# Kernel tuning notes

Measured on AMD Instinct MI355X. Metric: run time of the kernel, lower is better.

Reference implementation:

```python
import jax, jax.numpy as jnp
import numpy as np

DIM = 1024
NUM_HEADS = 16
HEAD_DIM = DIM // NUM_HEADS
HIDDEN = 2 * DIM  # swiglu hidden


def rotate_half(x):
    x1, x2 = jnp.split(x, 2, axis=-1)
    return jnp.concatenate((-x2, x1), axis=-1)


def setup_inputs() -> dict:
    key = jax.random.key(0)
    ks = jax.random.split(key, 9)
    s = lambda fan_in: 1.0 / np.sqrt(fan_in)
    x = jax.random.normal(ks[0], (4, 2048, DIM), dtype=jnp.float32)
    qkv_w = jax.random.uniform(ks[1], (3 * DIM, DIM), minval=-s(DIM), maxval=s(DIM))
    proj_w = jax.random.uniform(ks[2], (DIM, DIM), minval=-s(DIM), maxval=s(DIM))
    proj_b = jax.random.uniform(ks[3], (DIM,), minval=-s(DIM), maxval=s(DIM))
    w1_w = jax.random.uniform(ks[4], (HIDDEN, DIM), minval=-s(DIM), maxval=s(DIM))
    w1_b = jnp.zeros((HIDDEN,), jnp.float32)
    w2_w = jax.random.uniform(ks[5], (HIDDEN, DIM), minval=-s(DIM), maxval=s(DIM))
    w2_b = jnp.zeros((HIDDEN,), jnp.float32)
    w3_w = jax.random.uniform(ks[6], (DIM, HIDDEN), minval=-s(HIDDEN), maxval=s(HIDDEN))
    w3_b = jnp.zeros((DIM,), jnp.float32)
    return {"x": x, "qkv_w": qkv_w, "proj_w": proj_w, "proj_b": proj_b,
            "w1_w": w1_w, "w1_b": w1_b, "w2_w": w2_w, "w2_b": w2_b,
            "w3_w": w3_w, "w3_b": w3_b}


def reference(x, qkv_w, proj_w, proj_b, w1_w, w1_b, w2_w, w2_b, w3_w, w3_b):
    B, N, C = x.shape
    H, D = NUM_HEADS, HEAD_DIM
    scale = D ** -0.5
    # QKV projection (no bias)
    qkv = jnp.einsum('bnc,fc->bnf', x, qkv_w).reshape(B, N, 3, H, D)
    qkv = jnp.transpose(qkv, (2, 0, 3, 1, 4))  # [3, B, H, N, D]
    q, k, v = qkv[0], qkv[1], qkv[2]
    # Rotary embeddings
    inv_freq = 1.0 / (10000.0 ** (jnp.arange(0, D, 2, dtype=jnp.float32) / D))
    t = jnp.arange(N, dtype=jnp.float32)
    freqs = jnp.einsum('i,j->ij', t, inv_freq)
    emb = jnp.concatenate((freqs, freqs), axis=-1)[None, None]  # [1,1,N,D]
    cos, sin = jnp.cos(emb), jnp.sin(emb)
    q = q * cos + rotate_half(q) * sin
    k = k * cos + rotate_half(k) * sin
    # Attention (non-causal, as in source)
    attn = jnp.einsum('bhnd,bhmd->bhnm', q, k) * scale
    attn = jax.nn.softmax(attn, axis=-1)
    out = jnp.einsum('bhnm,bhmd->bhnd', attn, v)
    out = jnp.transpose(out, (0, 2, 1, 3)).reshape(B, N, C)
    out = jnp.einsum('bnc,fc->bnf', out, proj_w) + proj_b
    # SwiGLU MLP
    x1 = jnp.einsum('bnc,fc->bnf', out, w1_w) + w1_b
    x2 = jnp.einsum('bnc,fc->bnf', out, w2_w) + w2_b
    hidden = jax.nn.silu(x1) * x2
    return jnp.einsum('bnh,fh->bnf', hidden, w3_w) + w3_b
```

## Files before the change

kernel.cpp:

```cpp
#include <hip/hip_runtime.h>
#include <hip/hip_bf16.h>
#include <math.h>


#define SEQ     2048
#define BATCH   4
#define NH      16
#define CDIM    1024
#define MROWS   8192

typedef __bf16 bf16x8 __attribute__((ext_vector_type(8)));
typedef float  floatx4 __attribute__((ext_vector_type(4)));
typedef float  floatx16 __attribute__((ext_vector_type(16)));
typedef unsigned int u32;

__device__ __forceinline__ unsigned short f2bf(float f) {
    __bf16 h = (__bf16)f;
    return __builtin_bit_cast(unsigned short, h);
}
__device__ __forceinline__ float fexp2(float x) {
    float r; asm("v_exp_f32 %0, %1" : "=v"(r) : "v"(x)); return r;
}
__device__ __forceinline__ float frcp(float x) {
    float r; asm("v_rcp_f32 %0, %1" : "=v"(r) : "v"(x)); return r;
}
__device__ __forceinline__ u32 cvtpk(float lo, float hi) {
    u32 w; asm("v_cvt_pk_bf16_f32 %0, %1, %2" : "=v"(w) : "v"(lo), "v"(hi));
    return w;
}
__device__ __forceinline__ floatx4 mfma16(bf16x8 a, bf16x8 b, floatx4 c) {
    return __builtin_amdgcn_mfma_f32_16x16x32_bf16(a, b, c, 0, 0, 0);
}
__device__ __forceinline__ floatx16 mfma32(bf16x8 a, bf16x8 b, floatx16 c) {
    return __builtin_amdgcn_mfma_f32_32x32x16_bf16(a, b, c, 0, 0, 0);
}
__device__ __forceinline__ void gld16(void* lds, const void* g) {
    __builtin_amdgcn_global_load_lds(
        (const __attribute__((address_space(1))) u32*)g,
        (__attribute__((address_space(3))) u32*)lds, 16, 0, 0);
}
__device__ __forceinline__ void wait_vm0_barrier() {
    asm volatile("s_waitcnt vmcnt(0)" ::: "memory");
    __builtin_amdgcn_s_barrier();
    __builtin_amdgcn_sched_barrier(0);
}
__device__ __forceinline__ void raw_barrier() {
    __builtin_amdgcn_s_barrier();
    __builtin_amdgcn_sched_barrier(0);
}

template <int OUTMODE, bool BIAS>
__global__ __launch_bounds__(256) void mgemm(
    const unsigned short* __restrict__ A,
    const unsigned short* __restrict__ B,
    const float* __restrict__ bias,
    void* __restrict__ C, int ldc,
    int K)
{
    __shared__ __align__(16) unsigned short As[2][128 * 32];
    __shared__ __align__(16) unsigned short Bs[2][128 * 32];

    const int tid  = threadIdx.x;
    const int lane = tid & 63;
    const int wave = tid >> 6;
    const int l16  = lane & 15;
    const int quad = lane >> 4;
    const int wm = (wave >> 1) * 64, wn = (wave & 1) * 64;
    const int bm = blockIdx.y, bn = blockIdx.x;

    const unsigned short* Ag = A + (size_t)(bm * 128) * K;
    const unsigned short* Bg = B + (size_t)(bn * 128) * K;

    const int srow0 = wave * 32 + (lane >> 2);
    const int scol  = 8 * ((lane & 3) ^ ((lane >> 3) & 3));
    const unsigned short* gA0 = Ag + (size_t)srow0 * K + scol;
    const unsigned short* gA1 = Ag + (size_t)(srow0 + 16) * K + scol;
    const unsigned short* gB0 = Bg + (size_t)srow0 * K + scol;
    const unsigned short* gB1 = Bg + (size_t)(srow0 + 16) * K + scol;

    auto stage = [&](int b, int kt) {
        gld16(&As[b][(wave * 2 + 0) * 512], gA0 + kt);
        gld16(&As[b][(wave * 2 + 1) * 512], gA1 + kt);
        gld16(&Bs[b][(wave * 2 + 0) * 512], gB0 + kt);
        gld16(&Bs[b][(wave * 2 + 1) * 512], gB1 + kt);
    };

    const int qsw = (quad ^ ((l16 >> 1) & 3)) * 8;

    floatx4 acc[4][4] = {};
    const int NK = K >> 5;

    stage(0, 0);
    wait_vm0_barrier();

    for (int i = 0; i < NK; ++i) {
        const int cur = i & 1;
        if (i + 1 < NK) stage(cur ^ 1, (i + 1) * 32);

        bf16x8 af[4], bfr[4];
        #pragma unroll
        for (int mt = 0; mt < 4; ++mt)
            af[mt] = *(const bf16x8*)&As[cur][(wm + mt * 16 + l16) * 32 + qsw];
        #pragma unroll
        for (int nt = 0; nt < 4; ++nt)
            bfr[nt] = *(const bf16x8*)&Bs[cur][(wn + nt * 16 + l16) * 32 + qsw];
        #pragma unroll
        for (int mt = 0; mt < 4; ++mt)
            #pragma unroll
            for (int nt = 0; nt < 4; ++nt)
                acc[mt][nt] = mfma16(af[mt], bfr[nt], acc[mt][nt]);

        if (i + 1 < NK) wait_vm0_barrier();
        else            raw_barrier();
    }

    #pragma unroll
    for (int nt = 0; nt < 4; ++nt) {
        const int gcol = bn * 128 + wn + nt * 16 + l16;
        const float bv = BIAS ? bias[gcol] : 0.0f;
        #pragma unroll
        for (int mt = 0; mt < 4; ++mt) {
            #pragma unroll
            for (int r = 0; r < 4; ++r) {
                const int grow = bm * 128 + wm + mt * 16 + quad * 4 + r;
                float v = acc[mt][nt][r] + bv;
                if (OUTMODE == 0)
                    ((float*)C)[(size_t)grow * ldc + gcol] = v;
                else
                    ((unsigned short*)C)[(size_t)grow * ldc + gcol] = f2bf(v);
            }
        }
    }
}

#define RD_A(buf, mh)                                                     \
    { _Pragma("unroll") for (int i_ = 0; i_ < 4; ++i_) {                  \
        const int ro_ = (arow + ((mh) * 4 + i_) * 16) * 64;               \
        aF[i_][0] = *(const bf16x8*)&As[buf][ro_ + e0];                   \
        aF[i_][1] = *(const bf16x8*)&As[buf][ro_ + e1]; } }

#define RD_B(buf, nh)                                                     \
    { _Pragma("unroll") for (int n_ = 0; n_ < 2; ++n_) {                  \
        const int ro_ = (brow + ((nh) * 2 + n_) * 16) * 64;               \
        bF[nh][n_][0] = *(const bf16x8*)&Bs[buf][ro_ + e0];               \
        bF[nh][n_][1] = *(const bf16x8*)&Bs[buf][ro_ + e1]; } }

#define DO_MFMA(mh, nh)                                                   \
    { _Pragma("unroll") for (int i_ = 0; i_ < 4; ++i_)                    \
      { _Pragma("unroll") for (int n_ = 0; n_ < 2; ++n_) {                \
        acc[(mh)*4+i_][(nh)*2+n_] =                                       \
            mfma16(aF[i_][0], bF[nh][n_][0], acc[(mh)*4+i_][(nh)*2+n_]);  \
        acc[(mh)*4+i_][(nh)*2+n_] =                                       \
            mfma16(aF[i_][1], bF[nh][n_][1], acc[(mh)*4+i_][(nh)*2+n_]);  \
      } } }

#define PH_ENTER()                                                        \
    __builtin_amdgcn_s_barrier();                                         \
    asm volatile("s_waitcnt lgkmcnt(0)" ::: "memory");                    \
    __builtin_amdgcn_sched_barrier(0);                                    \
    __builtin_amdgcn_s_setprio(1)

#define PH_EXIT() __builtin_amdgcn_s_setprio(0)

#define EIGHT_PHASE_LOOP()                                                \
    stA(0, 0, 0); stA(0, 1, 0); stB(0, 0, 0); stB(0, 1, 0);               \
    stA(1, 0, 64);                                                        \
    asm volatile("s_waitcnt vmcnt(2)" ::: "memory");                      \
    __builtin_amdgcn_s_barrier();                                         \
    __builtin_amdgcn_sched_barrier(0);                                    \
    for (int j = 0; j < 8; ++j) {                                         \
        const int k1 = (2 * j + 1) * 64;                                  \
        const int k2 = (2 * j + 2) * 64;                                  \
        const int k3 = (2 * j + 3) * 64;                                  \
        const bool more = (j < 7);                                        \
        RD_A(0, 0); RD_B(0, 0);                                           \
        stA(1, 1, k1);                                                    \
        PH_ENTER(); DO_MFMA(0, 0); PH_EXIT();                             \
        __builtin_amdgcn_s_barrier();                                     \
        RD_B(0, 1);                                                       \
        stB(1, 0, k1);                                                    \
        PH_ENTER(); DO_MFMA(0, 1); PH_EXIT();                             \
        __builtin_amdgcn_s_barrier();                                     \
        RD_A(0, 1);                                                       \
        stB(1, 1, k1);                                                    \
        PH_ENTER(); DO_MFMA(1, 1); PH_EXIT();                             \
        __builtin_amdgcn_s_barrier();                                     \
        if (more) stA(0, 0, k2);                                          \
        PH_ENTER(); DO_MFMA(1, 0); PH_EXIT();                             \
        if (more) { asm volatile("s_waitcnt vmcnt(2)" ::: "memory"); }    \
        else      { asm volatile("s_waitcnt vmcnt(0)" ::: "memory"); }    \
        __builtin_amdgcn_s_barrier();                                     \
        RD_A(1, 0); RD_B(1, 0);                                           \
        if (more) stA(0, 1, k2);                                          \
        PH_ENTER(); DO_MFMA(0, 0); PH_EXIT();                             \
        __builtin_amdgcn_s_barrier();                                     \
        RD_B(1, 1);                                                       \
        if (more) stB(0, 0, k2);                                          \
        PH_ENTER(); DO_MFMA(0, 1); PH_EXIT();                             \
        __builtin_amdgcn_s_barrier();                                     \
        RD_A(1, 1);                                                       \
        if (more) stB(0, 1, k2);                                          \
        PH_ENTER(); DO_MFMA(1, 1); PH_EXIT();                             \
        __builtin_amdgcn_s_barrier();                                     \
        if (more) stA(1, 0, k3);                                          \
        PH_ENTER(); DO_MFMA(1, 0); PH_EXIT();                             \
        if (more) {                                                       \
            asm volatile("s_waitcnt vmcnt(2)" ::: "memory");              \
            __builtin_amdgcn_s_barrier();                                 \
        }                                                                 \
    }

__global__ __launch_bounds__(512, 2) void mgemm_glu(
    const unsigned short* __restrict__ B1p,
    const unsigned short* __restrict__ B2p,
    const unsigned short* __restrict__ A,
    const float* __restrict__ bias1,
    const float* __restrict__ bias2,
    unsigned short* __restrict__ C, int ldc)
{
    __shared__ __align__(16) unsigned short As[2][256 * 64];
    __shared__ __align__(16) unsigned short Bs[2][256 * 64];

    const int tid  = threadIdx.x;
    const int lane = tid & 63;
    const int wave = tid >> 6;
    const int l16  = lane & 15;
    const int quad = lane >> 4;
    const int wr   = wave >> 2;
    const int wc   = wave & 3;
    const int bn = blockIdx.x, bm = blockIdx.y;
    const int K = CDIM;

    const unsigned short* Ag = A + (size_t)(bm * 256) * K;

    const int srow  = lane >> 3;
    const int sgcol = ((lane & 7) ^ srow) * 8;

    auto stA = [&](int buf, int half, int kt) {
        #pragma unroll
        for (int s = 0; s < 2; ++s) {
            const int rbase = half * 128 + (wave * 2 + s) * 8;
            gld16(&As[buf][rbase * 64],
                  Ag + (size_t)(rbase + srow) * K + kt + sgcol);
        }
    };
    auto stB = [&](int buf, int half, int kt) {
        #pragma unroll
        for (int s = 0; s < 2; ++s) {
            const int rbase = half * 128 + (wave * 2 + s) * 8;
            const int q = rbase >> 6, r6 = rbase & 63;
            const unsigned short* src = (r6 < 32)
                ? B1p + (size_t)(bn * 128 + q * 32 + r6) * K
                : B2p + (size_t)(bn * 128 + q * 32 + (r6 - 32)) * K;
            gld16(&Bs[buf][rbase * 64],
                  src + (size_t)srow * K + kt + sgcol);
        }
    };

    const int e0 = ((quad)     ^ (l16 & 7)) * 8;
    const int e1 = ((quad + 4) ^ (l16 & 7)) * 8;
    const int arow = wr * 128 + l16;
    const int brow = wc * 64 + l16;

    floatx4 acc[8][4] = {};
    bf16x8 aF[4][2];
    bf16x8 bF[2][2][2];

    EIGHT_PHASE_LOOP();

    #pragma unroll
    for (int nt = 0; nt < 2; ++nt) {
        const int gcol = bn * 128 + wc * 32 + nt * 16 + l16;
        const float b1 = bias1[gcol];
        const float b2 = bias2[gcol];
        #pragma unroll
        for (int m = 0; m < 8; ++m) {
            #pragma unroll
            for (int r = 0; r < 4; ++r) {
                const int grow = bm * 256 + wr * 128 + m * 16 + quad * 4 + r;
                const float x1 = acc[m][nt][r] + b1;
                const float x2 = acc[m][nt + 2][r] + b2;
                const float e = fexp2(x1 * -1.44269504088896f);
                const float v = x1 * frcp(1.0f + e) * x2;
                C[(size_t)grow * ldc + gcol] = f2bf(v);
            }
        }
    }
}

__global__ __launch_bounds__(512, 2) void mgemm_qkv(
    const unsigned short* __restrict__ A,
    const unsigned short* __restrict__ B,
    const float* __restrict__ tab,
    unsigned short* __restrict__ Qb,
    unsigned short* __restrict__ Kb,
    unsigned short* __restrict__ Vtb)
{
    __shared__ __align__(16) unsigned short As[2][256 * 64];
    __shared__ __align__(16) unsigned short Bs[2][256 * 64];

    const int tid  = threadIdx.x;
    const int lane = tid & 63;
    const int wave = tid >> 6;
    const int l16  = lane & 15;
    const int quad = lane >> 4;
    const int wr   = wave >> 2;
    const int wc   = wave & 3;
    const int bn = blockIdx.x, bm = blockIdx.y;
    const int K = CDIM;

    const unsigned short* Ag = A + (size_t)(bm * 256) * K;
    const unsigned short* Bg = B + (size_t)(bn * 256) * K;

    const int srow  = lane >> 3;
    const int sgcol = ((lane & 7) ^ srow) * 8;

    auto stA = [&](int buf, int half, int kt) {
        #pragma unroll
        for (int s = 0; s < 2; ++s) {
            const int rbase = half * 128 + (wave * 2 + s) * 8;
            gld16(&As[buf][rbase * 64],
                  Ag + (size_t)(rbase + srow) * K + kt + sgcol);
        }
    };
    auto stB = [&](int buf, int half, int kt) {
        #pragma unroll
        for (int s = 0; s < 2; ++s) {
            const int rbase = half * 128 + (wave * 2 + s) * 8;
            gld16(&Bs[buf][rbase * 64],
                  Bg + (size_t)(rbase + srow) * K + kt + sgcol);
        }
    };

    const int e0 = ((quad)     ^ (l16 & 7)) * 8;
    const int e1 = ((quad + 4) ^ (l16 & 7)) * 8;
    const int arow = wr * 128 + l16;
    const int brow = wc * 64 + l16;

    floatx4 acc[8][4] = {};
    bf16x8 aF[4][2];
    bf16x8 bF[2][2][2];

    EIGHT_PHASE_LOOP();

    const int part = bn >> 2;

    if (part == 2) {
        unsigned short* T = &As[0][0];
        #pragma unroll
        for (int m = 0; m < 8; ++m) {
            __syncthreads();
            #pragma unroll
            for (int n = 0; n < 4; ++n) {
                ushort4 pk;
                pk.x = f2bf(acc[m][n][0]); pk.y = f2bf(acc[m][n][1]);
                pk.z = f2bf(acc[m][n][2]); pk.w = f2bf(acc[m][n][3]);
                *(ushort4*)&T[(wr * 256 + wc * 64 + n * 16 + l16) * 16 + quad * 4] = pk;
            }
            __syncthreads();
            const int wr2 = tid >> 8, col = tid & 255;
            const int grow0 = bm * 256 + wr2 * 128 + m * 16;
            const int b = grow0 >> 11, n0 = grow0 & 2047;
            const int h2 = (bn & 3) * 4 + (col >> 6);
            const int d  = col & 63;
            unsigned short* dst = Vtb +
                ((size_t)(b * NH + h2) * 64 + d) * 2048 + n0;
            const int tb = (wr2 * 256 + col) * 16;
            *(uint4*)dst       = *(const uint4*)&T[tb];
            *(uint4*)(dst + 8) = *(const uint4*)&T[tb + 8];
        }
    } else {
        const float qscale = (part == 0) ? 0.125f * 1.44269504088896f : 1.0f;
        const int h = (bn & 3) * 4 + wc;
        unsigned short* qk = (part == 0) ? Qb : Kb;
        #pragma unroll
        for (int m = 0; m < 8; ++m) {
            #pragma unroll
            for (int r = 0; r < 4; ++r) {
                const int grow = bm * 256 + wr * 128 + m * 16 + quad * 4 + r;
                const int b = grow >> 11, n = grow & 2047;
                unsigned short* dst = qk + ((size_t)(b * NH + h) * 2048 + n) * 64;
                #pragma unroll
                for (int nt = 0; nt < 2; ++nt) {
                    const int i = nt * 16 + l16;
                    const float c  = tab[(n * 32 + i) * 2];
                    const float sn = tab[(n * 32 + i) * 2 + 1];
                    const float x1  = acc[m][nt][r];
                    const float x2v = acc[m][nt + 2][r];
                    dst[i]      = f2bf((x1 * c - x2v * sn) * qscale);
                    dst[i + 32] = f2bf((x2v * c + x1 * sn) * qscale);
                }
            }
        }
    }
}

__global__ __launch_bounds__(256) void attn_mfma(
    const unsigned short* __restrict__ Qb,
    const unsigned short* __restrict__ Kb,
    const unsigned short* __restrict__ Vtb,
    unsigned short* __restrict__ Ob)
{
    const int bh = blockIdx.x;
    const int qt = blockIdx.y;
    const int tid = threadIdx.x;
    const int lane = tid & 63, wave = tid >> 6;
    const int r32 = lane & 31, hi = lane >> 5;
    const int qrow = wave * 32 + r32;

    __shared__ unsigned short QP[128][72];
    __shared__ unsigned short Ks[64][72];
    __shared__ unsigned short Vs[64][72];

    const unsigned short* Qg = Qb + ((size_t)bh * 2048 + qt * 128) * 64;
    const unsigned short* Kg = Kb + (size_t)bh * 2048 * 64;
    const unsigned short* Vg = Vtb + (size_t)bh * 64 * 2048;

    #pragma unroll
    for (int rep = 0; rep < 4; ++rep) {
        const int c = tid + rep * 256;
        const int r = c >> 3, d0 = (c & 7) * 8;
        *(uint4*)&QP[r][d0] = *(const uint4*)(Qg + (size_t)r * 64 + d0);
    }

    const int c0 = tid, c1 = tid + 256;
    const int kr0 = c0 >> 3, kd0 = (c0 & 7) * 8;
    const int kr1 = c1 >> 3, kd1 = (c1 & 7) * 8;

    uint4 ka0 = *(const uint4*)(Kg + (size_t)kr0 * 64 + kd0);
    uint4 ka1 = *(const uint4*)(Kg + (size_t)kr1 * 64 + kd1);
    uint4 va0 = *(const uint4*)(Vg + (size_t)kr0 * 2048 + kd0);
    uint4 va1 = *(const uint4*)(Vg + (size_t)kr1 * 2048 + kd1);

    __syncthreads();

    bf16x8 bq[4];
    #pragma unroll
    for (int f = 0; f < 4; ++f)
        bq[f] = *(const bf16x8*)&QP[qrow][f * 16 + hi * 8];

    floatx16 o0 = {}, o1 = {};
    float l_acc = 0.0f;

    for (int kt = 0; kt < 32; ++kt) {
        __syncthreads();
        *(uint4*)&Ks[kr0][kd0] = ka0;
        *(uint4*)&Ks[kr1][kd1] = ka1;
        *(uint4*)&Vs[kr0][kd0] = va0;
        *(uint4*)&Vs[kr1][kd1] = va1;
        if (kt + 1 < 32) {
            const size_t nb = (size_t)(kt + 1) * 64;
            ka0 = *(const uint4*)(Kg + (nb + kr0) * 64 + kd0);
            ka1 = *(const uint4*)(Kg + (nb + kr1) * 64 + kd1);
            va0 = *(const uint4*)(Vg + (size_t)kr0 * 2048 + nb + kd0);
            va1 = *(const uint4*)(Vg + (size_t)kr1 * 2048 + nb + kd1);
        }
        __syncthreads();

        #pragma unroll
        for (int t = 0; t < 2; ++t) {
            floatx16 s = {};
            #pragma unroll
            for (int f = 0; f < 4; ++f) {
                const bf16x8 ak = *(const bf16x8*)&Ks[t * 32 + r32][f * 16 + hi * 8];
                s = mfma32(ak, bq[f], s);
            }
            float p[16];
            float rs = 0.0f;
            #pragma unroll
            for (int g = 0; g < 16; ++g) { p[g] = fexp2(s[g]); rs += p[g]; }
            l_acc += rs;
            u32 w0 = cvtpk(p[0], p[1]),   w2 = cvtpk(p[4], p[5]);
            u32 w1 = cvtpk(p[2], p[3]),   w3 = cvtpk(p[6], p[7]);
            u32 w4 = cvtpk(p[8], p[9]),   w6 = cvtpk(p[12], p[13]);
            u32 w5 = cvtpk(p[10], p[11]), w7 = cvtpk(p[14], p[15]);
            asm("v_permlane32_swap_b32 %0, %1" : "+v"(w0), "+v"(w2));
            asm("v_permlane32_swap_b32 %0, %1" : "+v"(w1), "+v"(w3));
            asm("v_permlane32_swap_b32 %0, %1" : "+v"(w4), "+v"(w6));
            asm("v_permlane32_swap_b32 %0, %1" : "+v"(w5), "+v"(w7));
            uint4 u0; u0.x = w0; u0.y = w1; u0.z = w2; u0.w = w3;
            uint4 u1; u1.x = w4; u1.y = w5; u1.z = w6; u1.w = w7;
            const bf16x8 bp0 = __builtin_bit_cast(bf16x8, u0);
            const bf16x8 bp1 = __builtin_bit_cast(bf16x8, u1);
            {
                const int f0 = 2 * t, f1 = 2 * t + 1;
                const bf16x8 av00 = *(const bf16x8*)&Vs[r32][f0 * 16 + hi * 8];
                const bf16x8 av01 = *(const bf16x8*)&Vs[32 + r32][f0 * 16 + hi * 8];
                o0 = mfma32(av00, bp0, o0);
                o1 = mfma32(av01, bp0, o1);
                const bf16x8 av10 = *(const bf16x8*)&Vs[r32][f1 * 16 + hi * 8];
                const bf16x8 av11 = *(const bf16x8*)&Vs[32 + r32][f1 * 16 + hi * 8];
                o0 = mfma32(av10, bp1, o0);
                o1 = mfma32(av11, bp1, o1);
            }
        }
    }

    const float l_tot = l_acc + __shfl_xor(l_acc, 32);
    const float inv = 1.0f / l_tot;
    const int b = bh >> 4, h = bh & 15;
    unsigned short* orow = Ob +
        (size_t)(b * SEQ + qt * 128 + qrow) * CDIM + h * 64;
    #pragma unroll
    for (int u = 0; u < 2; ++u) {
        const floatx16 ov = u ? o1 : o0;
        #pragma unroll
        for (int g = 0; g < 4; ++g) {
            ushort4 pk;
            pk.x = f2bf(ov[4 * g + 0] * inv); pk.y = f2bf(ov[4 * g + 1] * inv);
            pk.z = f2bf(ov[4 * g + 2] * inv); pk.w = f2bf(ov[4 * g + 3] * inv);
            *(ushort4*)(orow + u * 32 + 8 * g + 4 * hi) = pk;
        }
    }
}

__global__ __launch_bounds__(256) void cvt_all(
    const float* __restrict__ x,    const float* __restrict__ qkv,
    const float* __restrict__ proj, const float* __restrict__ w1,
    const float* __restrict__ w2,   const float* __restrict__ w3,
    unsigned short* __restrict__ xb,    unsigned short* __restrict__ qkvb,
    unsigned short* __restrict__ projb, unsigned short* __restrict__ w1b,
    unsigned short* __restrict__ w2b,   unsigned short* __restrict__ w3b)
{
    const size_t i = ((size_t)blockIdx.x * 256 + threadIdx.x) * 4;
    const float* src; unsigned short* dst; size_t off;
    if      (i <  8388608) { src = x;    dst = xb;    off = 0; }
    else if (i < 11534336) { src = qkv;  dst = qkvb;  off = 8388608; }
    else if (i < 12582912) { src = proj; dst = projb; off = 11534336; }
    else if (i < 14680064) { src = w1;   dst = w1b;   off = 12582912; }
    else if (i < 16777216) { src = w2;   dst = w2b;   off = 14680064; }
    else                   { src = w3;   dst = w3b;   off = 16777216; }
    const size_t j = i - off;
    const float4 f = *(const float4*)(src + j);
    ushort4 o; o.x = f2bf(f.x); o.y = f2bf(f.y); o.z = f2bf(f.z); o.w = f2bf(f.w);
    *(ushort4*)(dst + j) = o;
}

__global__ __launch_bounds__(256) void rope_table(float* __restrict__ tab)
{
    const int idx = blockIdx.x * 256 + threadIdx.x;
    const int i = idx & 31, n = idx >> 5;
    const double f = (double)n * pow(10000.0, -(double)(2 * i) / 64.0);
    tab[idx * 2]     = (float)cos(f);
    tab[idx * 2 + 1] = (float)sin(f);
}

extern "C" void kernel_launch(void* const* d_in, const int* in_sizes, int n_in,
                              void* d_out, int out_size, void* d_ws, size_t ws_size,
                              hipStream_t stream)
{
    const float* x      = (const float*)d_in[0];
    const float* qkv_w  = (const float*)d_in[1];
    const float* proj_w = (const float*)d_in[2];
    const float* proj_b = (const float*)d_in[3];
    const float* w1_w   = (const float*)d_in[4];
    const float* w1_b   = (const float*)d_in[5];
    const float* w2_w   = (const float*)d_in[6];
    const float* w2_b   = (const float*)d_in[7];
    const float* w3_w   = (const float*)d_in[8];
    const float* w3_b   = (const float*)d_in[9];
    float* out = (float*)d_out;

    char* ws = (char*)d_ws;
    unsigned short* Qb    = (unsigned short*)(ws);
    unsigned short* Kb    = (unsigned short*)(ws + 16777216);
    unsigned short* Vtb   = (unsigned short*)(ws + 33554432);
    unsigned short* Ob    = (unsigned short*)(ws + 50331648);
    unsigned short* out1b = (unsigned short*)(ws + 67108864);
    unsigned short* w1b   = (unsigned short*)(ws + 83886080);
    unsigned short* w2b   = (unsigned short*)(ws + 88080384);
    unsigned short* w3b   = (unsigned short*)(ws + 92274688);
    unsigned short* projb = (unsigned short*)(ws + 96468992);
    unsigned short* xb    = (unsigned short*)(ws + 98566144);
    unsigned short* wqkvb = (unsigned short*)(ws + 115343360);
    float*          tab   = (float*)(ws + 121634816);
    unsigned short* hid   = (unsigned short*)(ws);

    const dim3 blk(256);

    cvt_all<<<dim3(18432), blk, 0, stream>>>(
        x, qkv_w, proj_w, w1_w, w2_w, w3_w,
        xb, wqkvb, projb, w1b, w2b, w3b);
    rope_table<<<dim3(256), blk, 0, stream>>>(tab);

    mgemm_qkv<<<dim3(12, 32), dim3(512), 0, stream>>>(xb, wqkvb, tab, Qb, Kb, Vtb);
    attn_mfma<<<dim3(BATCH * NH, SEQ / 128), blk, 0, stream>>>(Qb, Kb, Vtb, Ob);
    mgemm<1, true><<<dim3(8, 64), blk, 0, stream>>>(
        Ob, projb, proj_b, out1b, CDIM, CDIM);
    mgemm_glu<<<dim3(16, 32), dim3(512), 0, stream>>>(
        w1b, w2b, out1b, w1_b, w2_b, hid, 2048);
    mgemm<0, true><<<dim3(8, 64), blk, 0, stream>>>(
        hid, w3b, w3_b, out, CDIM, 2048);
}
```

Measured before the change: 422.8 us.

## Port proj and w3 GEMMs to 8-wave eight-phase pipelined kernel

Replaces the simple double-buffered 128x128 mgemm used for the output projection and final w3 GEMM with a 512-thread 256x128 tile kernel. The new kernel reuses the eight-phase staged-load/MFMA schedule already used by the GLU and QKV GEMMs, now with a configurable K trip count. The aim is to hide global-to-LDS latency and raise MFMA density. Separately, the attention kernel swaps __syncthreads for an explicit lgkmcnt wait plus barrier and raises wave priority around its MFMA groups. The larger tile halves the grid to 256 blocks, which may underfill the GPU's compute units.

```diff
diff --git a/kernel.cpp b/kernel.cpp
--- a/kernel.cpp
+++ b/kernel.cpp
@@ -39,99 +39,62 @@
         (const __attribute__((address_space(1))) u32*)g,
         (__attribute__((address_space(3))) u32*)lds, 16, 0, 0);
 }
-__device__ __forceinline__ void wait_vm0_barrier() {
-    asm volatile("s_waitcnt vmcnt(0)" ::: "memory");
-    __builtin_amdgcn_s_barrier();
-    __builtin_amdgcn_sched_barrier(0);
-}
-__device__ __forceinline__ void raw_barrier() {
-    __builtin_amdgcn_s_barrier();
-    __builtin_amdgcn_sched_barrier(0);
-}
-
-template <int OUTMODE, bool BIAS>
-__global__ __launch_bounds__(256) void mgemm(
-    const unsigned short* __restrict__ A,
-    const unsigned short* __restrict__ B,
-    const float* __restrict__ bias,
-    void* __restrict__ C, int ldc,
-    int K)
-{
-    __shared__ __align__(16) unsigned short As[2][128 * 32];
-    __shared__ __align__(16) unsigned short Bs[2][128 * 32];
-
-    const int tid  = threadIdx.x;
-    const int lane = tid & 63;
-    const int wave = tid >> 6;
-    const int l16  = lane & 15;
-    const int quad = lane >> 4;
-    const int wm = (wave >> 1) * 64, wn = (wave & 1) * 64;
-    const int bm = blockIdx.y, bn = blockIdx.x;
-
-    const unsigned short* Ag = A + (size_t)(bm * 128) * K;
-    const unsigned short* Bg = B + (size_t)(bn * 128) * K;
-
-    const int srow0 = wave * 32 + (lane >> 2);
-    const int scol  = 8 * ((lane & 3) ^ ((lane >> 3) & 3));
-    const unsigned short* gA0 = Ag + (size_t)srow0 * K + scol;
-    const unsigned short* gA1 = Ag + (size_t)(srow0 + 16) * K + scol;
-    const unsigned short* gB0 = Bg + (size_t)srow0 * K + scol;
-    const unsigned short* gB1 = Bg + (size_t)(srow0 + 16) * K + scol;
-
-    auto stage = [&](int b, int kt) {
-        gld16(&As[b][(wave * 2 + 0) * 512], gA0 + kt);
-        gld16(&As[b][(wave * 2 + 1) * 512], gA1 + kt);
-        gld16(&Bs[b][(wave * 2 + 0) * 512], gB0 + kt);
-        gld16(&Bs[b][(wave * 2 + 1) * 512], gB1 + kt);
-    };
-
-    const int qsw = (quad ^ ((l16 >> 1) & 3)) * 8;
-
-    floatx4 acc[4][4] = {};
-    const int NK = K >> 5;
-
-    stage(0, 0);
-    wait_vm0_barrier();
-
-    for (int i = 0; i < NK; ++i) {
-        const int cur = i & 1;
-        if (i + 1 < NK) stage(cur ^ 1, (i + 1) * 32);
-
-        bf16x8 af[4], bfr[4];
-        #pragma unroll
-        for (int mt = 0; mt < 4; ++mt)
-            af[mt] = *(const bf16x8*)&As[cur][(wm + mt * 16 + l16) * 32 + qsw];
-        #pragma unroll
-        for (int nt = 0; nt < 4; ++nt)
-            bfr[nt] = *(const bf16x8*)&Bs[cur][(wn + nt * 16 + l16) * 32 + qsw];
-        #pragma unroll
-        for (int mt = 0; mt < 4; ++mt)
-            #pragma unroll
-            for (int nt = 0; nt < 4; ++nt)
-                acc[mt][nt] = mfma16(af[mt], bfr[nt], acc[mt][nt]);
-
-        if (i + 1 < NK) wait_vm0_barrier();
-        else            raw_barrier();
-    }
-
-    #pragma unroll
-    for (int nt = 0; nt < 4; ++nt) {
-        const int gcol = bn * 128 + wn + nt * 16 + l16;
-        const float bv = BIAS ? bias[gcol] : 0.0f;
-        #pragma unroll
-        for (int mt = 0; mt < 4; ++mt) {
-            #pragma unroll
-            for (int r = 0; r < 4; ++r) {
-                const int grow = bm * 128 + wm + mt * 16 + quad * 4 + r;
-                float v = acc[mt][nt][r] + bv;
-                if (OUTMODE == 0)
-                    ((float*)C)[(size_t)grow * ldc + gcol] = v;
-                else
-                    ((unsigned short*)C)[(size_t)grow * ldc + gcol] = f2bf(v);
-            }
-        }
-    }
-}
+
+#define PH_ENTER()                                                        \
+    __builtin_amdgcn_s_barrier();                                         \
+    asm volatile("s_waitcnt lgkmcnt(0)" ::: "memory");                    \
+    __builtin_amdgcn_sched_barrier(0);                                    \
+    __builtin_amdgcn_s_setprio(1)
+
+#define PH_EXIT() __builtin_amdgcn_s_setprio(0)
+
+#define EIGHT_PHASE_LOOP(NJ)                                              \
+    stA(0, 0, 0); stA(0, 1, 0); stB(0, 0, 0); stB(0, 1, 0);               \
+    stA(1, 0, 64);                                                        \
+    asm volatile("s_waitcnt vmcnt(2)" ::: "memory");                      \
+    __builtin_amdgcn_s_barrier();                                         \
+    __builtin_amdgcn_sched_barrier(0);                                    \
+    for (int j = 0; j < (NJ); ++j) {                                      \
+        const int k1 = (2 * j + 1) * 64;                                  \
+        const int k2 = (2 * j + 2) * 64;                                  \
+        const int k3 = (2 * j + 3) * 64;                                  \
+        const bool more = (j < (NJ) - 1);                                 \
+        RD_A(0, 0); RD_B(0, 0);                                           \
+        stA(1, 1, k1);                                                    \
+        PH_ENTER(); DO_MFMA(0, 0); PH_EXIT();                             \
+        __builtin_amdgcn_s_barrier();                                     \
+        RD_B(0, 1);                                                       \
+        stB(1, 0, k1);                                                    \
+        PH_ENTER(); DO_MFMA(0, 1); PH_EXIT();                             \
+        __builtin_amdgcn_s_barrier();                                     \
+        RD_A(0, 1);                                                       \
+        stB(1, 1, k1);                                                    \
+        PH_ENTER(); DO_MFMA(1, 1); PH_EXIT();                             \
+        __builtin_amdgcn_s_barrier();                                     \
+        if (more) stA(0, 0, k2);                                          \
+        PH_ENTER(); DO_MFMA(1, 0); PH_EXIT();                             \
+        if (more) { asm volatile("s_waitcnt vmcnt(2)" ::: "memory"); }    \
+        else      { asm volatile("s_waitcnt vmcnt(0)" ::: "memory"); }    \
+        __builtin_amdgcn_s_barrier();                                     \
+        RD_A(1, 0); RD_B(1, 0);                                           \
+        if (more) stA(0, 1, k2);                                          \
+        PH_ENTER(); DO_MFMA(0, 0); PH_EXIT();                             \
+        __builtin_amdgcn_s_barrier();                                     \
+        RD_B(1, 1);                                                       \
+        if (more) stB(0, 0, k2);                                          \
+        PH_ENTER(); DO_MFMA(0, 1); PH_EXIT();                             \
+        __builtin_amdgcn_s_barrier();                                     \
+        RD_A(1, 1);                                                       \
+        if (more) stB(0, 1, k2);                                          \
+        PH_ENTER(); DO_MFMA(1, 1); PH_EXIT();                             \
+        __builtin_amdgcn_s_barrier();                                     \
+        if (more) stA(1, 0, k3);                                          \
+        PH_ENTER(); DO_MFMA(1, 0); PH_EXIT();                             \
+        if (more) {                                                       \
+            asm volatile("s_waitcnt vmcnt(2)" ::: "memory");              \
+            __builtin_amdgcn_s_barrier();                                 \
+        }                                                                 \
+    }
 
 #define RD_A(buf, mh)                                                     \
     { _Pragma("unroll") for (int i_ = 0; i_ < 4; ++i_) {                  \
@@ -153,62 +116,6 @@
         acc[(mh)*4+i_][(nh)*2+n_] =                                       \
             mfma16(aF[i_][1], bF[nh][n_][1], acc[(mh)*4+i_][(nh)*2+n_]);  \
       } } }
-
-#define PH_ENTER()                                                        \
-    __builtin_amdgcn_s_barrier();                                         \
-    asm volatile("s_waitcnt lgkmcnt(0)" ::: "memory");                    \
-    __builtin_amdgcn_sched_barrier(0);                                    \
-    __builtin_amdgcn_s_setprio(1)
-
-#define PH_EXIT() __builtin_amdgcn_s_setprio(0)
-
-#define EIGHT_PHASE_LOOP()                                                \
-    stA(0, 0, 0); stA(0, 1, 0); stB(0, 0, 0); stB(0, 1, 0);               \
-    stA(1, 0, 64);                                                        \
-    asm volatile("s_waitcnt vmcnt(2)" ::: "memory");                      \
-    __builtin_amdgcn_s_barrier();                                         \
-    __builtin_amdgcn_sched_barrier(0);                                    \
-    for (int j = 0; j < 8; ++j) {                                         \
-        const int k1 = (2 * j + 1) * 64;                                  \
-        const int k2 = (2 * j + 2) * 64;                                  \
-        const int k3 = (2 * j + 3) * 64;                                  \
-        const bool more = (j < 7);                                        \
-        RD_A(0, 0); RD_B(0, 0);                                           \
-        stA(1, 1, k1);                                                    \
-        PH_ENTER(); DO_MFMA(0, 0); PH_EXIT();                             \
-        __builtin_amdgcn_s_barrier();                                     \
-        RD_B(0, 1);                                                       \
-        stB(1, 0, k1);                                                    \
-        PH_ENTER(); DO_MFMA(0, 1); PH_EXIT();                             \
-        __builtin_amdgcn_s_barrier();                                     \
-        RD_A(0, 1);                                                       \
-        stB(1, 1, k1);                                                    \
-        PH_ENTER(); DO_MFMA(1, 1); PH_EXIT();                             \
-        __builtin_amdgcn_s_barrier();                                     \
-        if (more) stA(0, 0, k2);                                          \
-        PH_ENTER(); DO_MFMA(1, 0); PH_EXIT();                             \
-        if (more) { asm volatile("s_waitcnt vmcnt(2)" ::: "memory"); }    \
-        else      { asm volatile("s_waitcnt vmcnt(0)" ::: "memory"); }    \
-        __builtin_amdgcn_s_barrier();                                     \
-        RD_A(1, 0); RD_B(1, 0);                                           \
-        if (more) stA(0, 1, k2);                                          \
-        PH_ENTER(); DO_MFMA(0, 0); PH_EXIT();                             \
-        __builtin_amdgcn_s_barrier();                                     \
-        RD_B(1, 1);                                                       \
-        if (more) stB(0, 0, k2);                                          \
-        PH_ENTER(); DO_MFMA(0, 1); PH_EXIT();                             \
-        __builtin_amdgcn_s_barrier();                                     \
-        RD_A(1, 1);                                                       \
-        if (more) stB(0, 1, k2);                                          \
-        PH_ENTER(); DO_MFMA(1, 1); PH_EXIT();                             \
-        __builtin_amdgcn_s_barrier();                                     \
-        if (more) stA(1, 0, k3);                                          \
-        PH_ENTER(); DO_MFMA(1, 0); PH_EXIT();                             \
-        if (more) {                                                       \
-            asm volatile("s_waitcnt vmcnt(2)" ::: "memory");              \
-            __builtin_amdgcn_s_barrier();                                 \
-        }                                                                 \
-    }
 
 __global__ __launch_bounds__(512, 2) void mgemm_glu(
     const unsigned short* __restrict__ B1p,
@@ -266,7 +173,7 @@
     bf16x8 aF[4][2];
     bf16x8 bF[2][2][2];
 
-    EIGHT_PHASE_LOOP();
+    EIGHT_PHASE_LOOP(8);
 
     #pragma unroll
     for (int nt = 0; nt < 2; ++nt) {
@@ -341,7 +248,7 @@
     bf16x8 aF[4][2];
     bf16x8 bF[2][2][2];
 
-    EIGHT_PHASE_LOOP();
+    EIGHT_PHASE_LOOP(8);
 
     const int part = bn >> 2;
 
@@ -395,6 +302,91 @@
     }
 }
 
+#undef RD_B
+#undef DO_MFMA
+#define RD_B(buf, nh)                                                     \
+    { const int ro_ = (brow + (nh) * 16) * 64;                            \
+      bF[nh][0] = *(const bf16x8*)&Bs[buf][ro_ + e0];                     \
+      bF[nh][1] = *(const bf16x8*)&Bs[buf][ro_ + e1]; }
+
+#define DO_MFMA(mh, nh)                                                   \
+    { _Pragma("unroll") for (int i_ = 0; i_ < 4; ++i_) {                  \
+        acc[(mh)*4+i_][nh] =                                              \
+            mfma16(aF[i_][0], bF[nh][0], acc[(mh)*4+i_][nh]);             \
+        acc[(mh)*4+i_][nh] =                                              \
+            mfma16(aF[i_][1], bF[nh][1], acc[(mh)*4+i_][nh]); } }
+
+template <int OUTMODE, bool BIAS>
+__global__ __launch_bounds__(512, 2) void mgemm8(
+    const unsigned short* __restrict__ A,
+    const unsigned short* __restrict__ B,
+    const float* __restrict__ bias,
+    void* __restrict__ C, int ldc,
+    int K)
+{
+    __shared__ __align__(16) unsigned short As[2][256 * 64];
+    __shared__ __align__(16) unsigned short Bs[2][128 * 64];
+
+    const int tid  = threadIdx.x;
+    const int lane = tid & 63;
+    const int wave = tid >> 6;
+    const int l16  = lane & 15;
+    const int quad = lane >> 4;
+    const int wr   = wave >> 2;
+    const int wc   = wave & 3;
+    const int bn = blockIdx.x, bm = blockIdx.y;
+
+    const unsigned short* Ag = A + (size_t)(bm * 256) * K;
+    const unsigned short* Bg = B + (size_t)(bn * 128) * K;
+
+    const int srow  = lane >> 3;
+    const int sgcol = ((lane & 7) ^ srow) * 8;
+
+    auto stA = [&](int buf, int half, int kt) {
+        #pragma unroll
+        for (int s = 0; s < 2; ++s) {
+            const int rbase = half * 128 + (wave * 2 + s) * 8;
+            gld16(&As[buf][rbase * 64],
+                  Ag + (size_t)(rbase + srow) * K + kt + sgcol);
+        }
+    };
+    auto stB = [&](int buf, int half, int kt) {
+        const int rbase = half * 64 + wave * 8;
+        gld16(&Bs[buf][rbase * 64],
+              Bg + (size_t)(rbase + srow) * K + kt + sgcol);
+    };
+
+    const int e0 = ((quad)     ^ (l16 & 7)) * 8;
+    const int e1 = ((quad + 4) ^ (l16 & 7)) * 8;
+    const int arow = wr * 128 + l16;
+    const int brow = wc * 32 + l16;
+
+    floatx4 acc[8][2] = {};
+    bf16x8 aF[4][2];
+    bf16x8 bF[2][2];
+
+    const int NJ = K >> 7;
+    EIGHT_PHASE_LOOP(NJ);
+
+    #pragma unroll
+    for (int nt = 0; nt < 2; ++nt) {
+        const int gcol = bn * 128 + wc * 32 + nt * 16 + l16;
+        const float bv = BIAS ? bias[gcol] : 0.0f;
+        #pragma unroll
+        for (int m = 0; m < 8; ++m) {
+            #pragma unroll
+            for (int r = 0; r < 4; ++r) {
+                const int grow = bm * 256 + wr * 128 + m * 16 + quad * 4 + r;
+                float v = acc[m][nt][r] + bv;
+                if (OUTMODE == 0)
+                    ((float*)C)[(size_t)grow * ldc + gcol] = v;
+                else
+                    ((unsigned short*)C)[(size_t)grow * ldc + gcol] = f2bf(v);
+            }
+        }
+    }
+}
+
 __global__ __launch_bounds__(256) void attn_mfma(
     const unsigned short* __restrict__ Qb,
     const unsigned short* __restrict__ Kb,
@@ -455,16 +447,20 @@
             va0 = *(const uint4*)(Vg + (size_t)kr0 * 2048 + nb + kd0);
             va1 = *(const uint4*)(Vg + (size_t)kr1 * 2048 + nb + kd1);
         }
-        __syncthreads();
+        asm volatile("s_waitcnt lgkmcnt(0)" ::: "memory");
+        __builtin_amdgcn_s_barrier();
+        __builtin_amdgcn_sched_barrier(0);
 
         #pragma unroll
         for (int t = 0; t < 2; ++t) {
             floatx16 s = {};
+            __builtin_amdgcn_s_setprio(1);
             #pragma unroll
             for (int f = 0; f < 4; ++f) {
                 const bf16x8 ak = *(const bf16x8*)&Ks[t * 32 + r32][f * 16 + hi * 8];
                 s = mfma32(ak, bq[f], s);
             }
+            __builtin_amdgcn_s_setprio(0);
             float p[16];
             float rs = 0.0f;
             #pragma unroll
@@ -486,12 +482,16 @@
                 const int f0 = 2 * t, f1 = 2 * t + 1;
                 const bf16x8 av00 = *(const bf16x8*)&Vs[r32][f0 * 16 + hi * 8];
                 const bf16x8 av01 = *(const bf16x8*)&Vs[32 + r32][f0 * 16 + hi * 8];
+                __builtin_amdgcn_s_setprio(1);
                 o0 = mfma32(av00, bp0, o0);
                 o1 = mfma32(av01, bp0, o1);
+                __builtin_amdgcn_s_setprio(0);
                 const bf16x8 av10 = *(const bf16x8*)&Vs[r32][f1 * 16 + hi * 8];
                 const bf16x8 av11 = *(const bf16x8*)&Vs[32 + r32][f1 * 16 + hi * 8];
+                __builtin_amdgcn_s_setprio(1);
                 o0 = mfma32(av10, bp1, o0);
                 o1 = mfma32(av11, bp1, o1);
+                __builtin_amdgcn_s_setprio(0);
             }
         }
     }
@@ -585,10 +585,10 @@
 
     mgemm_qkv<<<dim3(12, 32), dim3(512), 0, stream>>>(xb, wqkvb, tab, Qb, Kb, Vtb);
     attn_mfma<<<dim3(BATCH * NH, SEQ / 128), blk, 0, stream>>>(Qb, Kb, Vtb, Ob);
-    mgemm<1, true><<<dim3(8, 64), blk, 0, stream>>>(
+    mgemm8<1, true><<<dim3(8, 32), dim3(512), 0, stream>>>(
         Ob, projb, proj_b, out1b, CDIM, CDIM);
     mgemm_glu<<<dim3(16, 32), dim3(512), 0, stream>>>(
         w1b, w2b, out1b, w1_b, w2_b, hid, 2048);
-    mgemm<0, true><<<dim3(8, 64), blk, 0, stream>>>(
+    mgemm8<0, true><<<dim3(8, 32), dim3(512), 0, stream>>>(
         hid, w3b, w3_b, out, CDIM, 2048);
 }
```

Measured after the change: 436.2 us. +3.2%, slower.
